# Optimization experiments

Hardware: AMD Instinct MI355X
Metric: run time of the kernel (lower is better)

## Reference

```python
import jax, jax.numpy as jnp
import numpy as np

B, L, C = 8, 256, 64
NEG = -1e30  # large negative instead of -inf to keep grads NaN-free


def setup_inputs() -> dict:
    key = jax.random.key(0)
    k1, k2 = jax.random.split(key)
    scores = jax.random.normal(k1, (B, L, L, C), dtype=jnp.float32)
    lens = jax.random.randint(k2, (B,), 64, L, dtype=jnp.int32)  # sentence lengths in [64, L-1]
    return {"scores": scores, "lens": lens}


def _inside_max(scores, lens):
    """Max-semiring CKY inside pass. scores: [B,L,L,C]; returns logZ per batch [B]."""
    t = jnp.transpose(jnp.max(scores, axis=-1), (1, 2, 0))  # [L,L,B] best label per span
    s0 = jnp.zeros((L, L, B), scores.dtype)                 # chart s[i,j] = best score of span (i,j)
    i = jnp.arange(L)
    j = jnp.arange(L)

    def step(s, w):
        e = jnp.clip(i + w, 0, L - 1)                       # span end, [L]
        k = jnp.clip(i[:, None] + j[None, :], 0, L - 1)     # split points, [L,L]
        left = s[i[:, None], k]                             # s[i, i+j], [L,L,B]
        right = s[k, e[:, None]]                            # s[i+j, i+w], [L,L,B]
        valid = (j[None, :] >= 1) & (j[None, :] < w) & ((i + w) < L)[:, None]
        comb = jnp.max(jnp.where(valid[..., None], left + right, NEG), axis=1)  # [L,B]
        s_l = t[i, e]                                       # label-max span score, [L,B]
        diag = jnp.where(w == 1, s_l, comb + s_l)
        row_ok = ((i + w) < L)[:, None]
        upd = jnp.where(row_ok, diag, s[i, e])
        s = s.at[i, e].set(upd)
        return s, None

    s, _ = jax.lax.scan(step, s0, jnp.arange(1, L))
    lens_c = jnp.clip(lens, 1, L - 1)
    return s[0, lens_c, jnp.arange(B)]                      # logZ (best tree score) per sentence


def reference(scores, lens):
    return _inside_max(scores, lens)
```

## Files before the change

kernel.cpp:

```cpp
#include <hip/hip_runtime.h>

#define LVAL 256
#define T    32
#define ST   36
#define SLAB (T * ST)
#define NB   8
#define NEG  (-1e30f)

typedef float f32x4 __attribute__((ext_vector_type(4)));

#define SOFT_FENCE() asm volatile("" ::: "memory")

__device__ __forceinline__ size_t sidx(int b, int i, int e) {
    return ((size_t)b << 16) + (i << 8) + e;
}

__device__ __forceinline__ void st_coh4(float* p, f32x4 v) {
    asm volatile("global_store_dwordx4 %0, %1, off sc0 sc1"
                 :: "v"(p), "v"(v) : "memory");
}
__device__ __forceinline__ f32x4 ld_coh4(const float* p) {
    f32x4 v;
    asm volatile("global_load_dwordx4 %0, %1, off sc0 sc1\n\t"
                 "s_waitcnt vmcnt(0)"
                 : "=&v"(v) : "v"(p) : "memory");
    return v;
}
__device__ __forceinline__ void ld_coh4x4(const float* p,
                                          f32x4& a, f32x4& b, f32x4& c, f32x4& d) {
    asm volatile("global_load_dwordx4 %0, %4, off sc0 sc1\n\t"
                 "global_load_dwordx4 %1, %4, off offset:16 sc0 sc1\n\t"
                 "global_load_dwordx4 %2, %4, off offset:32 sc0 sc1\n\t"
                 "global_load_dwordx4 %3, %4, off offset:48 sc0 sc1\n\t"
                 "s_waitcnt vmcnt(0)"
                 : "=&v"(a), "=&v"(b), "=&v"(c), "=&v"(d)
                 : "v"(p) : "memory");
}

template<int CTRL>
__device__ __forceinline__ float dpp_max(float v) {
#if __has_builtin(__builtin_amdgcn_mov_dpp)
    int o = __builtin_amdgcn_mov_dpp(__builtin_bit_cast(int, v), CTRL, 0xF, 0xF, true);
    return fmaxf(v, __builtin_bit_cast(float, o));
#else
    return fmaxf(v, __shfl_xor(v, CTRL == 0xB1 ? 1 : 2));
#endif
}

__global__ __launch_bounds__(256) void phase1(const float* __restrict__ scores,
                                              float* __restrict__ s,
                                              int* __restrict__ bar) {
    if (blockIdx.x == 0 && blockIdx.y == 0) {
        for (int k = threadIdx.x; k < 2048; k += 256) bar[k] = 0;
    }
    const int i = blockIdx.x, b = blockIdx.y;
    const int sub = threadIdx.x & 15, slot = threadIdx.x >> 4;
    const float* row = scores + ((((size_t)b * LVAL + i) * LVAL) << 6);
    #pragma unroll 4
    for (int m0 = 0; m0 < LVAL; m0 += 16) {
        const int e = m0 + slot;
        if (e > i) {
            float4 v = *((const float4*)(row + ((size_t)e << 6)) + sub);
            float mx = fmaxf(fmaxf(v.x, v.y), fmaxf(v.z, v.w));
            #pragma unroll
            for (int d = 1; d < 16; d <<= 1) mx = fmaxf(mx, __shfl_xor(mx, d));
            if (sub == 0) s[sidx(b, i, e)] = mx;
        }
    }
}

template<int LP>
__device__ __forceinline__ void diag_step(int lane, int l,
                                          float (*cur)[ST], float (*curT)[ST],
                                          const float (*tb)[ST]) {
    const int cells = T - l;
    const int P = 1 << LP;
    const int c = lane >> LP, p = lane & (P - 1);
    const bool guard = c < cells;
    const int li = guard ? c : 0;
    const int le = guard ? c + l : 0;
    constexpr int NF = 8 >> LP;
    const float tv = tb[li][le];
    float acc = NEG;
    #pragma unroll
    for (int m = 0; m < NF; ++m) {
        const int k0 = 4 * (p + m * P);
        float4 cu = *(const float4*)&cur[li][k0];
        float4 ct = *(const float4*)&curT[le][k0];
        acc = fmaxf(acc, fmaxf(fmaxf(cu.x + ct.x, cu.y + ct.y),
                               fmaxf(cu.z + ct.z, cu.w + ct.w)));
    }
    acc = dpp_max<0xB1>(acc);
    if (LP >= 2) acc = dpp_max<0x4E>(acc);
    const float v = acc + tv;
    if (guard && p == 0) cur[li][le] = v;
    if (guard && p == 1) curT[le][li] = v;
}

template<int LP>
__device__ __forceinline__ void edge_step(int lane, int l, int D,
                                          const float (*Ae)[ST], const float (*BeT)[ST],
                                          float (*cur)[ST], float (*curT)[ST],
                                          const float (*tb)[ST], const float (*pre)[ST]) {
    const int delta = l - (T - 1);
    const int ad = delta < 0 ? -delta : delta;
    const int cells = T - ad;
    const int P = 1 << LP;
    const int c = lane >> LP, p = lane & (P - 1);
    const bool guard = c < cells;
    const int li = guard ? (delta < 0 ? c + ad : c) : 0;
    const int le = guard ? li + delta : 0;
    constexpr int NF = 8 >> LP;
    const float tv = tb[li][le];
    float acc = pre[li][le];
    #pragma unroll
    for (int m = 0; m < NF; ++m) {
        const int k0 = 4 * (p + m * P);
        float4 a  = *(const float4*)&Ae[li][k0];
        float4 ct = *(const float4*)&curT[le][k0];
        float4 cu = *(const float4*)&cur[li][k0];
        float4 bt = *(const float4*)&BeT[le][k0];
        float s0 = fmaxf(fmaxf(a.x + ct.x, a.y + ct.y), fmaxf(a.z + ct.z, a.w + ct.w));
        float s1 = fmaxf(fmaxf(cu.x + bt.x, cu.y + bt.y), fmaxf(cu.z + bt.z, cu.w + bt.w));
        acc = fmaxf(acc, fmaxf(s0, s1));
    }
    acc = dpp_max<0xB1>(acc);
    if (LP >= 2) acc = dpp_max<0x4E>(acc);
    const float v = (D == 1 && l == 0) ? tv : acc + tv;
    if (guard && p == 0) cur[li][le] = v;
    if (guard && p == 1) curT[le][li] = v;
}

__device__ __forceinline__ void gemm_blk(const float* ATs, const float (*BW)[ST],
                                         int r0, int c0, float (&ag)[4][4]) {
    const float (*AT)[ST] = (const float(*)[ST])ATs;
    #pragma unroll 4
    for (int k = 0; k < T; ++k) {
        f32x4 a4 = *(const f32x4*)&AT[k][r0];
        f32x4 b4 = *(const f32x4*)&BW[k][c0];
        #pragma unroll
        for (int i = 0; i < 4; ++i)
            #pragma unroll
            for (int j = 0; j < 4; ++j)
                ag[i][j] = fmaxf(ag[i][j], a4[i] + b4[j]);
    }
}

__device__ __forceinline__ void batch_barrier(int* __restrict__ bar, int b,
                                              int tid, int ep) {
    asm volatile("s_waitcnt vmcnt(0)" ::: "memory");
    __syncthreads();
    if (tid == 0) {
        int* cnt  = bar + b * 256;
        int* flag = bar + b * 256 + 64;
        int prev = __hip_atomic_fetch_add(cnt, 1, __ATOMIC_RELAXED,
                                          __HIP_MEMORY_SCOPE_AGENT);
        if ((prev & (NB - 1)) == NB - 1) {
            __hip_atomic_store(flag, ep, __ATOMIC_RELAXED, __HIP_MEMORY_SCOPE_AGENT);
        } else {
            int guard = 0;
            while (__hip_atomic_load(flag, __ATOMIC_RELAXED,
                                     __HIP_MEMORY_SCOPE_AGENT) < ep) {
                __builtin_amdgcn_s_sleep(2);
                if (++guard > (1 << 22)) break;
            }
        }
    }
    __syncthreads();
}

__global__ __launch_bounds__(256) void dp_fused(float* __restrict__ s,
                                                const int* __restrict__ lens,
                                                float* __restrict__ out,
                                                int* __restrict__ bar) {
    __shared__ __align__(16) float smem[14 * SLAB];
    float* ATb = smem;
    float (*Ae)[ST]  = (float(*)[ST])(smem + 6 * SLAB);
    float (*tb)[ST]  = (float(*)[ST])(smem + 7 * SLAB);
    float (*BeT)[ST] = (float(*)[ST])(smem + 8 * SLAB);
    float (*cur)[ST] = (float(*)[ST])(smem + 9 * SLAB);
    float* BWb = smem + 10 * SLAB;
    float (*pre)[ST] = (float(*)[ST])BWb;

    const int b  = blockIdx.x & 7;
    const int bi = blockIdx.x >> 3;
    const int tid = threadIdx.x, wid = tid >> 6, lane = tid & 63;
    const int lr = tid >> 5, lc = tid & 31;
    const int grow = lane >> 1, gc = (lane & 1) * 16;
    const int gly = lane >> 3, glx = lane & 7, r0 = 4 * gly, c0 = 4 * glx;
    const int trow = tid >> 3, tc4 = (tid & 7) * 4;
    float (*BW)[ST] = (float(*)[ST])(BWb + wid * SLAB);

    f32x4 pbA[4], pbB[4];
    f32x4 tpb[4], bpb[4];

    if (wid == 0) {
        float (*curT0)[ST] = (float(*)[ST])(BWb + 1 * SLAB);
        float (*t0)[ST]    = (float(*)[ST])(BWb + 2 * SLAB);
        const float4 negv = make_float4(NEG, NEG, NEG, NEG);
        #pragma unroll
        for (int j = 0; j < 4; ++j) {
            float4 v = *(const float4*)&s[sidx(b, bi * T + grow, bi * T + gc + 4 * j)];
            *(float4*)&t0[grow][gc + 4 * j]    = v;
            *(float4*)&Ae[grow][gc + 4 * j]    = negv;
            *(float4*)&curT0[grow][gc + 4 * j] = negv;
        }
        SOFT_FENCE();
        if (lane < T - 1) {
            float v = t0[lane][lane + 1];
            Ae[lane][lane + 1] = v;
            curT0[lane + 1][lane] = v;
        }
        SOFT_FENCE();
        #pragma unroll 1
        for (int l = 2; l < T; ++l) {
            if (T - l <= 16) diag_step<2>(lane, l, Ae, curT0, t0);
            else             diag_step<1>(lane, l, Ae, curT0, t0);
            SOFT_FENCE();
        }
        #pragma unroll
        for (int j = 0; j < 4; ++j)
            st_coh4(&s[sidx(b, bi * T + grow, bi * T + gc + 4 * j)],
                    *(const f32x4*)&Ae[grow][gc + 4 * j]);
    } else if (bi + 1 < NB) {
        for (int idx = tid - 64; idx < 256; idx += 192) {
            const int row = idx >> 3, c4 = (idx & 7) * 4;
            *(float4*)&tb[row][c4] =
                *(const float4*)&s[sidx(b, bi * T + row, (bi + 1) * T + c4)];
        }
    }

    #pragma unroll 1
    for (int D = 1; D < NB; ++D) {
        batch_barrier(bar, b, tid, D);
        const int be = bi + D;
        if (be < NB) {
            if (D == 1) {
                f32x4 v = ld_coh4(&s[sidx(b, be * T + trow, be * T + tc4)]);
                BeT[tc4 + 0][trow] = (trow < tc4 + 0) ? v[0] : NEG;
                BeT[tc4 + 1][trow] = (trow < tc4 + 1) ? v[1] : NEG;
                BeT[tc4 + 2][trow] = (trow < tc4 + 2) ? v[2] : NEG;
                BeT[tc4 + 3][trow] = (trow < tc4 + 3) ? v[3] : NEG;
            }
            const int nw = (D - 1 < 4) ? (D - 1) : 4;
            float ag[4][4];
            #pragma unroll
            for (int i = 0; i < 4; ++i)
                #pragma unroll
                for (int j = 0; j < 4; ++j) ag[i][j] = NEG;
            if (D >= 2) {
                if (wid == 0) {
                    f32x4 b0, b1, b2, b3;
                    ld_coh4x4(&s[sidx(b, (bi + 1) * T + grow, be * T + gc)],
                              b0, b1, b2, b3);
                    *(f32x4*)&BW[grow][gc + 0]  = b0;
                    *(f32x4*)&BW[grow][gc + 4]  = b1;
                    *(f32x4*)&BW[grow][gc + 8]  = b2;
                    *(f32x4*)&BW[grow][gc + 12] = b3;
                    SOFT_FENCE();
                    gemm_blk(ATb + 0, BW, r0, c0, ag);
                } else {
                    if (wid <= D - 2) {
                        #pragma unroll
                        for (int j = 0; j < 4; ++j)
                            *(f32x4*)&BW[grow][gc + 4 * j] = pbA[j];
                        SOFT_FENCE();
                        gemm_blk(ATb + wid * SLAB, BW, r0, c0, ag);
                        SOFT_FENCE();
                    }
                    if (wid + 3 <= D - 2) {
                        #pragma unroll
                        for (int j = 0; j < 4; ++j)
                            *(f32x4*)&BW[grow][gc + 4 * j] = pbB[j];
                        SOFT_FENCE();
                        gemm_blk(ATb + (wid + 3) * SLAB, BW, r0, c0, ag);
                    }
                }
            }
            if (wid < nw) {
                #pragma unroll
                for (int i = 0; i < 4; ++i)
                    *(float4*)&BW[r0 + i][c0] =
                        make_float4(ag[i][0], ag[i][1], ag[i][2], ag[i][3]);
            }
            __syncthreads();
            #pragma unroll
            for (int r = 0; r < 4; ++r) {
                const int row = lr + 8 * r;
                float v = NEG;
                for (int w2 = 0; w2 < nw; ++w2)
                    v = fmaxf(v, BWb[w2 * SLAB + row * ST + lc]);
                pre[row][lc] = v;
            }
            __syncthreads();
            float (*curT)[ST] = (D == NB - 1) ? (float(*)[ST])(BWb + 1 * SLAB)
                                              : (float(*)[ST])(ATb + (D - 1) * SLAB);
            #pragma unroll
            for (int r = 0; r < 4; ++r) {
                const int row = lr + 8 * r;
                cur[row][lc]  = NEG;
                curT[row][lc] = NEG;
            }
            __syncthreads();
            if (wid == 0) {
                #pragma unroll 1
                for (int l = 0; l < 2 * T - 1; ++l) {
                    const int ad0 = (l < T - 1) ? (T - 1 - l) : (l - (T - 1));
                    if (ad0 >= 16) edge_step<2>(lane, l, D, Ae, BeT, cur, curT, tb, pre);
                    else           edge_step<1>(lane, l, D, Ae, BeT, cur, curT, tb, pre);
                    SOFT_FENCE();
                }
            } else if (be + 1 < NB) {
                if (wid <= D - 1)
                    ld_coh4x4(&s[sidx(b, (bi + 1 + wid) * T + grow, (be + 1) * T + gc)],
                              pbA[0], pbA[1], pbA[2], pbA[3]);
                if (wid + 3 <= D - 1)
                    ld_coh4x4(&s[sidx(b, (bi + 4 + wid) * T + grow, (be + 1) * T + gc)],
                              pbB[0], pbB[1], pbB[2], pbB[3]);
                if (wid == 1) {
                    #pragma unroll
                    for (int j = 0; j < 4; ++j)
                        tpb[j] = *(const f32x4*)&s[sidx(b, bi * T + grow,
                                                        (be + 1) * T + gc + 4 * j)];
                }
                if (wid == 2) {
                    #pragma unroll
                    for (int j = 0; j < 4; ++j)
                        bpb[j] = ld_coh4(&s[sidx(b, (be + 1) * T + grow,
                                                 (be + 1) * T + gc + 4 * j)]);
                }
            }
            __syncthreads();
            {
                f32x4 pv = *(const f32x4*)&cur[trow][tc4];
                st_coh4(&s[sidx(b, bi * T + trow, be * T + tc4)], pv);
            }
            if (be + 1 < NB) {
                if (wid == 1) {
                    #pragma unroll
                    for (int j = 0; j < 4; ++j)
                        *(f32x4*)&tb[grow][gc + 4 * j] = tpb[j];
                }
                if (wid == 2) {
                    #pragma unroll
                    for (int j = 0; j < 4; ++j)
                        #pragma unroll
                        for (int k = 0; k < 4; ++k) {
                            const int col = gc + 4 * j + k;
                            BeT[col][grow] = (grow < col) ? bpb[j][k] : NEG;
                        }
                }
            }
        }
    }

    if (bi == 0 && tid == 0) {
        int len = lens[b];
        len = len < 1 ? 1 : (len > LVAL - 1 ? LVAL - 1 : len);
        const int K = len >> 5, off = len & 31;
        float r;
        if (K == 0)           r = Ae[0][off];
        else if (K == NB - 1) r = cur[0][off];
        else                  r = ATb[(K - 1) * SLAB + off * ST];
        out[b] = r;
    }
}

extern "C" void kernel_launch(void* const* d_in, const int* in_sizes, int n_in,
                              void* d_out, int out_size, void* d_ws, size_t ws_size,
                              hipStream_t stream) {
    const float* scores = (const float*)d_in[0];
    const int*   lens   = (const int*)d_in[1];
    float*       out    = (float*)d_out;
    float*       s      = (float*)d_ws;
    int*         bar    = (int*)((char*)d_ws + ((size_t)(8) << 16) * sizeof(float));

    phase1<<<dim3(LVAL, 8), 256, 0, stream>>>(scores, s, bar);
    dp_fused<<<64, 256, 0, stream>>>(s, lens, out, bar);
}
```

Before: 341.0 us.

## Software-pipeline diagonal edge steps by precomputing the next anti-diagonal's partial max

The serial anti-diagonal loop over the diagonal block now computes most of step l+1's max-plus reduction early, while step l is still running. Only the single float4 chunk that can depend on the just-written cells is reloaded and reduced after the dependency resolves. The aim is to take shared-memory load latency off the serial 63-step critical chain. It also fixes two lanes per cell, dropping the four-lane variant. This adds register pressure and relies on a subtle argument that stale early reads fall only inside the recomputed chunk.

```diff
diff --git a/kernel.cpp b/kernel.cpp
--- a/kernel.cpp
+++ b/kernel.cpp
@@ -45,6 +45,20 @@
 #else
     return fmaxf(v, __shfl_xor(v, CTRL == 0xB1 ? 1 : 2));
 #endif
+}
+
+__device__ __forceinline__ float red8(const f32x4 a, const f32x4 b,
+                                      const f32x4 c, const f32x4 d) {
+    float m0 = fmaxf(a.x + b.x, a.y + b.y);
+    float m1 = fmaxf(a.z + b.z, a.w + b.w);
+    float m2 = fmaxf(c.x + d.x, c.y + d.y);
+    float m3 = fmaxf(c.z + d.z, c.w + d.w);
+    return fmaxf(fmaxf(m0, m1), fmaxf(m2, m3));
+}
+__device__ __forceinline__ float red4(const f32x4 a, const f32x4 b) {
+    float m0 = fmaxf(a.x + b.x, a.y + b.y);
+    float m1 = fmaxf(a.z + b.z, a.w + b.w);
+    return fmaxf(m0, m1);
 }
 
 __global__ __launch_bounds__(256) void phase1(const float* __restrict__ scores,
@@ -97,38 +111,30 @@
     if (guard && p == 1) curT[le][li] = v;
 }
 
-template<int LP>
-__device__ __forceinline__ void edge_step(int lane, int l, int D,
-                                          const float (*Ae)[ST], const float (*BeT)[ST],
-                                          float (*cur)[ST], float (*curT)[ST],
-                                          const float (*tb)[ST], const float (*pre)[ST]) {
+__device__ __forceinline__ void e_early(int l, int c, int p,
+        const float (*Ae)[ST], const float (*BeT)[ST],
+        const float (*cur)[ST], const float (*curT)[ST],
+        const float (*tb)[ST], const float (*pre)[ST],
+        float& accOut, float& tvOut, float& prOut) {
     const int delta = l - (T - 1);
     const int ad = delta < 0 ? -delta : delta;
     const int cells = T - ad;
-    const int P = 1 << LP;
-    const int c = lane >> LP, p = lane & (P - 1);
-    const bool guard = c < cells;
-    const int li = guard ? (delta < 0 ? c + ad : c) : 0;
-    const int le = guard ? li + delta : 0;
-    constexpr int NF = 8 >> LP;
-    const float tv = tb[li][le];
-    float acc = pre[li][le];
+    const bool g = c < cells;
+    const int li = g ? (delta < 0 ? c + ad : c) : 0;
+    const int le = g ? li + delta : 0;
+    tvOut = tb[li][le];
+    prOut = pre[li][le];
+    float acc = NEG;
     #pragma unroll
-    for (int m = 0; m < NF; ++m) {
-        const int k0 = 4 * (p + m * P);
-        float4 a  = *(const float4*)&Ae[li][k0];
-        float4 ct = *(const float4*)&curT[le][k0];
-        float4 cu = *(const float4*)&cur[li][k0];
-        float4 bt = *(const float4*)&BeT[le][k0];
-        float s0 = fmaxf(fmaxf(a.x + ct.x, a.y + ct.y), fmaxf(a.z + ct.z, a.w + ct.w));
-        float s1 = fmaxf(fmaxf(cu.x + bt.x, cu.y + bt.y), fmaxf(cu.z + bt.z, cu.w + bt.w));
-        acc = fmaxf(acc, fmaxf(s0, s1));
-    }
-    acc = dpp_max<0xB1>(acc);
-    if (LP >= 2) acc = dpp_max<0x4E>(acc);
-    const float v = (D == 1 && l == 0) ? tv : acc + tv;
-    if (guard && p == 0) cur[li][le] = v;
-    if (guard && p == 1) curT[le][li] = v;
+    for (int m = 0; m < 4; ++m) {
+        const int k0 = 4 * (p + 2 * m);
+        f32x4 a  = *(const f32x4*)&Ae[li][k0];
+        f32x4 ct = *(const f32x4*)&curT[le][k0];
+        f32x4 cu = *(const f32x4*)&cur[li][k0];
+        f32x4 bt = *(const f32x4*)&BeT[le][k0];
+        acc = fmaxf(acc, red8(a, ct, cu, bt));
+    }
+    accOut = acc;
 }
 
 __device__ __forceinline__ void gemm_blk(const float* ATs, const float (*BW)[ST],
@@ -190,6 +196,7 @@
     const int gly = lane >> 3, glx = lane & 7, r0 = 4 * gly, c0 = 4 * glx;
     const int trow = tid >> 3, tc4 = (tid & 7) * 4;
     float (*BW)[ST] = (float(*)[ST])(BWb + wid * SLAB);
+    const int c = lane >> 1, p = lane & 1;
 
     f32x4 pbA[4], pbB[4];
     f32x4 tpb[4], bpb[4];
@@ -280,8 +287,8 @@
             if (wid < nw) {
                 #pragma unroll
                 for (int i = 0; i < 4; ++i)
-                    *(float4*)&BW[r0 + i][c0] =
-                        make_float4(ag[i][0], ag[i][1], ag[i][2], ag[i][3]);
+                    *(f32x4*)&BW[r0 + i][c0] =
+                        f32x4{ag[i][0], ag[i][1], ag[i][2], ag[i][3]};
             }
             __syncthreads();
             #pragma unroll
@@ -303,12 +310,38 @@
             }
             __syncthreads();
             if (wid == 0) {
+                float accN, tvN, prN;
+                e_early(0, c, p, Ae, BeT, cur, curT, tb, pre, accN, tvN, prN);
+                SOFT_FENCE();
+                float accP = accN, tvC = tvN, prC = prN;
                 #pragma unroll 1
                 for (int l = 0; l < 2 * T - 1; ++l) {
-                    const int ad0 = (l < T - 1) ? (T - 1 - l) : (l - (T - 1));
-                    if (ad0 >= 16) edge_step<2>(lane, l, D, Ae, BeT, cur, curT, tb, pre);
-                    else           edge_step<1>(lane, l, D, Ae, BeT, cur, curT, tb, pre);
+                    const int delta = l - (T - 1);
+                    const int ad = delta < 0 ? -delta : delta;
+                    const int cells = T - ad;
+                    const bool g = c < cells;
+                    const int li = g ? (delta < 0 ? c + ad : c) : 0;
+                    const int le = g ? li + delta : 0;
+                    const int cfA = ((li + 1 < T ? li + 1 : T - 1) >> 2) << 2;
+                    const int cfB = ((le > 0 ? le - 1 : 0) >> 2) << 2;
+                    f32x4 lA  = *(const f32x4*)&Ae[li][cfA];
+                    f32x4 lCT = *(const f32x4*)&curT[le][cfA];
+                    f32x4 lCU = *(const f32x4*)&cur[li][cfB];
+                    f32x4 lBT = *(const f32x4*)&BeT[le][cfB];
                     SOFT_FENCE();
+                    if (l + 1 < 2 * T - 1)
+                        e_early(l + 1, c, p, Ae, BeT, cur, curT, tb, pre,
+                                accN, tvN, prN);
+                    SOFT_FENCE();
+                    float acc = fmaxf(accP, prC);
+                    acc = fmaxf(acc, red4(lA, lCT));
+                    acc = fmaxf(acc, red4(lCU, lBT));
+                    acc = dpp_max<0xB1>(acc);
+                    const float v = (D == 1 && l == 0) ? tvC : acc + tvC;
+                    if (g && p == 0) cur[li][le] = v;
+                    if (g && p == 1) curT[le][li] = v;
+                    SOFT_FENCE();
+                    accP = accN; tvC = tvN; prC = prN;
                 }
             } else if (be + 1 < NB) {
                 if (wid <= D - 1)
```

Measured after the change: 396.2 us. 16.2% more time.

## Replace per-batch global barrier with per-tile dataflow completion flags

Applied to the files above, without the earlier changes.

Drops the all-blocks-per-batch barrier at each anti-diagonal step. Each block now publishes a coherent flag when a tile (bi,be) is written and waits only for the specific tiles it depends on, so blocks can run ahead of the diagonal wavefront and idle blocks exit early. The B-tile prefetch into registers during the edge phase is removed; tiles are now loaded on demand after the dependency flags are seen. The cost is more spinning on flags and lost load/compute overlap, and the flags rely on zero-initialised workspace and guarded spin timeouts.

```diff
diff --git a/kernel.cpp b/kernel.cpp
--- a/kernel.cpp
+++ b/kernel.cpp
@@ -35,6 +35,23 @@
                  "s_waitcnt vmcnt(0)"
                  : "=&v"(a), "=&v"(b), "=&v"(c), "=&v"(d)
                  : "v"(p) : "memory");
+}
+__device__ __forceinline__ void st_coh1(int* p, int v) {
+    asm volatile("global_store_dword %0, %1, off sc0 sc1"
+                 :: "v"(p), "v"(v) : "memory");
+}
+__device__ __forceinline__ int ld_coh1(const int* p) {
+    int v;
+    asm volatile("global_load_dword %0, %1, off sc0 sc1\n\t"
+                 "s_waitcnt vmcnt(0)"
+                 : "=&v"(v) : "v"(p) : "memory");
+    return v;
+}
+__device__ __forceinline__ void spin_flag(int* f) {
+    int guard = 0;
+    while (ld_coh1(f) == 0) {
+        if (++guard > (1 << 20)) break;
+    }
 }
 
 template<int CTRL>
@@ -146,29 +163,6 @@
     }
 }
 
-__device__ __forceinline__ void batch_barrier(int* __restrict__ bar, int b,
-                                              int tid, int ep) {
-    asm volatile("s_waitcnt vmcnt(0)" ::: "memory");
-    __syncthreads();
-    if (tid == 0) {
-        int* cnt  = bar + b * 256;
-        int* flag = bar + b * 256 + 64;
-        int prev = __hip_atomic_fetch_add(cnt, 1, __ATOMIC_RELAXED,
-                                          __HIP_MEMORY_SCOPE_AGENT);
-        if ((prev & (NB - 1)) == NB - 1) {
-            __hip_atomic_store(flag, ep, __ATOMIC_RELAXED, __HIP_MEMORY_SCOPE_AGENT);
-        } else {
-            int guard = 0;
-            while (__hip_atomic_load(flag, __ATOMIC_RELAXED,
-                                     __HIP_MEMORY_SCOPE_AGENT) < ep) {
-                __builtin_amdgcn_s_sleep(2);
-                if (++guard > (1 << 22)) break;
-            }
-        }
-    }
-    __syncthreads();
-}
-
 __global__ __launch_bounds__(256) void dp_fused(float* __restrict__ s,
                                                 const int* __restrict__ lens,
                                                 float* __restrict__ out,
@@ -190,8 +184,8 @@
     const int gly = lane >> 3, glx = lane & 7, r0 = 4 * gly, c0 = 4 * glx;
     const int trow = tid >> 3, tc4 = (tid & 7) * 4;
     float (*BW)[ST] = (float(*)[ST])(BWb + wid * SLAB);
-
-    f32x4 pbA[4], pbB[4];
+    int* flags = bar + b * 64;
+
     f32x4 tpb[4], bpb[4];
 
     if (wid == 0) {
@@ -222,6 +216,8 @@
         for (int j = 0; j < 4; ++j)
             st_coh4(&s[sidx(b, bi * T + grow, bi * T + gc + 4 * j)],
                     *(const f32x4*)&Ae[grow][gc + 4 * j]);
+        asm volatile("s_waitcnt vmcnt(0)" ::: "memory");
+        if (lane == 0) st_coh1(&flags[bi * 8 + bi], 1);
     } else if (bi + 1 < NB) {
         for (int idx = tid - 64; idx < 256; idx += 192) {
             const int row = idx >> 3, c4 = (idx & 7) * 4;
@@ -231,125 +227,108 @@
     }
 
     #pragma unroll 1
-    for (int D = 1; D < NB; ++D) {
-        batch_barrier(bar, b, tid, D);
+    for (int D = 1; D <= NB - 1 - bi; ++D) {
         const int be = bi + D;
-        if (be < NB) {
-            if (D == 1) {
-                f32x4 v = ld_coh4(&s[sidx(b, be * T + trow, be * T + tc4)]);
-                BeT[tc4 + 0][trow] = (trow < tc4 + 0) ? v[0] : NEG;
-                BeT[tc4 + 1][trow] = (trow < tc4 + 1) ? v[1] : NEG;
-                BeT[tc4 + 2][trow] = (trow < tc4 + 2) ? v[2] : NEG;
-                BeT[tc4 + 3][trow] = (trow < tc4 + 3) ? v[3] : NEG;
-            }
-            const int nw = (D - 1 < 4) ? (D - 1) : 4;
-            float ag[4][4];
+        if (tid == 0) {
+            for (int K = bi + 1; K < be; ++K) spin_flag(&flags[K * 8 + be]);
+            if (D == 1) spin_flag(&flags[be * 8 + be]);
+        }
+        __syncthreads();
+        if (D == 1) {
+            f32x4 v = ld_coh4(&s[sidx(b, be * T + trow, be * T + tc4)]);
+            BeT[tc4 + 0][trow] = (trow < tc4 + 0) ? v[0] : NEG;
+            BeT[tc4 + 1][trow] = (trow < tc4 + 1) ? v[1] : NEG;
+            BeT[tc4 + 2][trow] = (trow < tc4 + 2) ? v[2] : NEG;
+            BeT[tc4 + 3][trow] = (trow < tc4 + 3) ? v[3] : NEG;
+        }
+        const int nw = (D - 1 < 4) ? (D - 1) : 4;
+        float ag[4][4];
+        #pragma unroll
+        for (int i = 0; i < 4; ++i)
+            #pragma unroll
+            for (int j = 0; j < 4; ++j) ag[i][j] = NEG;
+        for (int K = bi + 1 + wid; K < be; K += 4) {
+            const float (*AT)[ST] = (const float(*)[ST])(ATb + (K - bi - 1) * SLAB);
+            f32x4 b0, b1, b2, b3;
+            ld_coh4x4(&s[sidx(b, K * T + grow, be * T + gc)], b0, b1, b2, b3);
+            *(f32x4*)&BW[grow][gc + 0]  = b0;
+            *(f32x4*)&BW[grow][gc + 4]  = b1;
+            *(f32x4*)&BW[grow][gc + 8]  = b2;
+            *(f32x4*)&BW[grow][gc + 12] = b3;
+            SOFT_FENCE();
+            gemm_blk((const float*)AT, BW, r0, c0, ag);
+            SOFT_FENCE();
+        }
+        if (wid < nw) {
             #pragma unroll
             for (int i = 0; i < 4; ++i)
+                *(f32x4*)&BW[r0 + i][c0] =
+                    f32x4{ag[i][0], ag[i][1], ag[i][2], ag[i][3]};
+        }
+        __syncthreads();
+        #pragma unroll
+        for (int r = 0; r < 4; ++r) {
+            const int row = lr + 8 * r;
+            float v = NEG;
+            for (int w2 = 0; w2 < nw; ++w2)
+                v = fmaxf(v, BWb[w2 * SLAB + row * ST + lc]);
+            pre[row][lc] = v;
+        }
+        __syncthreads();
+        float (*curT)[ST] = (D == NB - 1) ? (float(*)[ST])(BWb + 1 * SLAB)
+                                          : (float(*)[ST])(ATb + (D - 1) * SLAB);
+        #pragma unroll
+        for (int r = 0; r < 4; ++r) {
+            const int row = lr + 8 * r;
+            cur[row][lc]  = NEG;
+            curT[row][lc] = NEG;
+        }
+        __syncthreads();
+        if (wid == 0) {
+            #pragma unroll 1
+            for (int l = 0; l < 2 * T - 1; ++l) {
+                const int ad0 = (l < T - 1) ? (T - 1 - l) : (l - (T - 1));
+                if (ad0 >= 16) edge_step<2>(lane, l, D, Ae, BeT, cur, curT, tb, pre);
+                else           edge_step<1>(lane, l, D, Ae, BeT, cur, curT, tb, pre);
+                SOFT_FENCE();
+            }
+        } else if (be + 1 < NB) {
+            if (wid == 1) {
                 #pragma unroll
-                for (int j = 0; j < 4; ++j) ag[i][j] = NEG;
-            if (D >= 2) {
-                if (wid == 0) {
-                    f32x4 b0, b1, b2, b3;
-                    ld_coh4x4(&s[sidx(b, (bi + 1) * T + grow, be * T + gc)],
-                              b0, b1, b2, b3);
-                    *(f32x4*)&BW[grow][gc + 0]  = b0;
-                    *(f32x4*)&BW[grow][gc + 4]  = b1;
-                    *(f32x4*)&BW[grow][gc + 8]  = b2;
-                    *(f32x4*)&BW[grow][gc + 12] = b3;
-                    SOFT_FENCE();
-                    gemm_blk(ATb + 0, BW, r0, c0, ag);
-                } else {
-                    if (wid <= D - 2) {
-                        #pragma unroll
-                        for (int j = 0; j < 4; ++j)
-                            *(f32x4*)&BW[grow][gc + 4 * j] = pbA[j];
-                        SOFT_FENCE();
-                        gemm_blk(ATb + wid * SLAB, BW, r0, c0, ag);
-                        SOFT_FENCE();
+                for (int j = 0; j < 4; ++j)
+                    tpb[j] = *(const f32x4*)&s[sidx(b, bi * T + grow,
+                                                    (be + 1) * T + gc + 4 * j)];
+            }
+            if (wid == 2) {
+                spin_flag(&flags[(be + 1) * 8 + (be + 1)]);
+                #pragma unroll
+                for (int j = 0; j < 4; ++j)
+                    bpb[j] = ld_coh4(&s[sidx(b, (be + 1) * T + grow,
+                                             (be + 1) * T + gc + 4 * j)]);
+            }
+        }
+        __syncthreads();
+        {
+            f32x4 pv = *(const f32x4*)&cur[trow][tc4];
+            st_coh4(&s[sidx(b, bi * T + trow, be * T + tc4)], pv);
+        }
+        asm volatile("s_waitcnt vmcnt(0)" ::: "memory");
+        __syncthreads();
+        if (tid == 0) st_coh1(&flags[bi * 8 + be], 1);
+        if (be + 1 < NB) {
+            if (wid == 1) {
+                #pragma unroll
+                for (int j = 0; j < 4; ++j)
+                    *(f32x4*)&tb[grow][gc + 4 * j] = tpb[j];
+            }
+            if (wid == 2) {
+                #pragma unroll
+                for (int j = 0; j < 4; ++j)
+                    #pragma unroll
+                    for (int k = 0; k < 4; ++k) {
+                        const int col = gc + 4 * j + k;
+                        BeT[col][grow] = (grow < col) ? bpb[j][k] : NEG;
                     }
-                    if (wid + 3 <= D - 2) {
-                        #pragma unroll
-                        for (int j = 0; j < 4; ++j)
-                            *(f32x4*)&BW[grow][gc + 4 * j] = pbB[j];
-                        SOFT_FENCE();
-                        gemm_blk(ATb + (wid + 3) * SLAB, BW, r0, c0, ag);
-                    }
-                }
-            }
-            if (wid < nw) {
-                #pragma unroll
-                for (int i = 0; i < 4; ++i)
-                    *(float4*)&BW[r0 + i][c0] =
-                        make_float4(ag[i][0], ag[i][1], ag[i][2], ag[i][3]);
-            }
-            __syncthreads();
-            #pragma unroll
-            for (int r = 0; r < 4; ++r) {
-                const int row = lr + 8 * r;
-                float v = NEG;
-                for (int w2 = 0; w2 < nw; ++w2)
-                    v = fmaxf(v, BWb[w2 * SLAB + row * ST + lc]);
-                pre[row][lc] = v;
-            }
-            __syncthreads();
-            float (*curT)[ST] = (D == NB - 1) ? (float(*)[ST])(BWb + 1 * SLAB)
-                                              : (float(*)[ST])(ATb + (D - 1) * SLAB);
-            #pragma unroll
-            for (int r = 0; r < 4; ++r) {
-                const int row = lr + 8 * r;
-                cur[row][lc]  = NEG;
-                curT[row][lc] = NEG;
-            }
-            __syncthreads();
-            if (wid == 0) {
-                #pragma unroll 1
-                for (int l = 0; l < 2 * T - 1; ++l) {
-                    const int ad0 = (l < T - 1) ? (T - 1 - l) : (l - (T - 1));
-                    if (ad0 >= 16) edge_step<2>(lane, l, D, Ae, BeT, cur, curT, tb, pre);
-                    else           edge_step<1>(lane, l, D, Ae, BeT, cur, curT, tb, pre);
-                    SOFT_FENCE();
-                }
-            } else if (be + 1 < NB) {
-                if (wid <= D - 1)
-                    ld_coh4x4(&s[sidx(b, (bi + 1 + wid) * T + grow, (be + 1) * T + gc)],
-                              pbA[0], pbA[1], pbA[2], pbA[3]);
-                if (wid + 3 <= D - 1)
-                    ld_coh4x4(&s[sidx(b, (bi + 4 + wid) * T + grow, (be + 1) * T + gc)],
-                              pbB[0], pbB[1], pbB[2], pbB[3]);
-                if (wid == 1) {
-                    #pragma unroll
-                    for (int j = 0; j < 4; ++j)
-                        tpb[j] = *(const f32x4*)&s[sidx(b, bi * T + grow,
-                                                        (be + 1) * T + gc + 4 * j)];
-                }
-                if (wid == 2) {
-                    #pragma unroll
-                    for (int j = 0; j < 4; ++j)
-                        bpb[j] = ld_coh4(&s[sidx(b, (be + 1) * T + grow,
-                                                 (be + 1) * T + gc + 4 * j)]);
-                }
-            }
-            __syncthreads();
-            {
-                f32x4 pv = *(const f32x4*)&cur[trow][tc4];
-                st_coh4(&s[sidx(b, bi * T + trow, be * T + tc4)], pv);
-            }
-            if (be + 1 < NB) {
-                if (wid == 1) {
-                    #pragma unroll
-                    for (int j = 0; j < 4; ++j)
-                        *(f32x4*)&tb[grow][gc + 4 * j] = tpb[j];
-                }
-                if (wid == 2) {
-                    #pragma unroll
-                    for (int j = 0; j < 4; ++j)
-                        #pragma unroll
-                        for (int k = 0; k < 4; ++k) {
-                            const int col = gc + 4 * j + k;
-                            BeT[col][grow] = (grow < col) ? bpb[j][k] : NEG;
-                        }
-                }
             }
         }
     }
```

Measured after the change: 339.1 us. About the same (-0.6%).
